# Kernel optimization log

Measured on AMD Instinct MI355X. Metric: run time of the kernel, lower is better.

Reference implementation:

```python
import jax, jax.numpy as jnp
import numpy as np

N = 400_000   # active voxels
CIN = 64
COUT = 64
D = 192       # dense bounding volume side
K = 27        # 3x3x3 kernel taps


def _build_kmap():
    """Build per-tap neighbor index map [27, N], -1 where neighbor voxel is inactive.
    Mirrors fvdb's SparseConvPackInfo for stride=1, kernel=3, out_grid == in_grid."""
    rng = np.random.default_rng(0)
    coords = rng.integers(0, D, size=(int(N * 1.6), 3), dtype=np.int64)
    lin = coords[:, 0] * D * D + coords[:, 1] * D + coords[:, 2]
    lin = np.unique(lin)[:N]
    assert lin.shape[0] == N
    coords = np.stack([lin // (D * D), (lin // D) % D, lin % D], axis=1)
    lookup = np.full(D * D * D, -1, np.int32)
    lookup[lin] = np.arange(N, dtype=np.int32)
    nbr = np.full((K, N), -1, np.int32)
    k = 0
    for a in (-1, 0, 1):
        for b in (-1, 0, 1):
            for c in (-1, 0, 1):
                nc = coords + np.array([a, b, c])
                valid = np.all((nc >= 0) & (nc < D), axis=1)
                nlin = nc[:, 0] * D * D + nc[:, 1] * D + nc[:, 2]
                nbr[k, valid] = lookup[nlin[valid]]
                k += 1
    return jnp.asarray(nbr)


def setup_inputs() -> dict:
    key = jax.random.key(0)
    k1, k2, k3 = jax.random.split(key, 3)
    std = 1.0 / np.sqrt(CIN * K)  # reset_parameters: uniform(-std, std)
    feats = jax.random.normal(k1, (N, CIN), jnp.float32)
    weight = jax.random.uniform(k2, (K, CIN, COUT), jnp.float32, -std, std)
    bias = jax.random.uniform(k3, (COUT,), jnp.float32, -std, std)
    return {"feats": feats, "weight": weight, "bias": bias, "nbr_idx": _build_kmap()}


def reference(feats, weight, bias, nbr_idx):
    # Gather-scatter sparse conv: out[j] = bias + sum_k feats[nbr_k(j)] @ W[k]
    safe_idx = jnp.maximum(nbr_idx, 0)          # [K, N]
    valid = nbr_idx >= 0                        # [K, N]
    out0 = jnp.broadcast_to(bias, (N, COUT)).astype(feats.dtype)

    def tap(carry, xs):
        idx, msk, w = xs                        # [N], [N], [CIN, COUT]
        g = jnp.where(msk[:, None], feats[idx], 0.0)  # masked gather [N, CIN]
        return carry + g @ w, None

    out, _ = jax.lax.scan(tap, out0, (safe_idx, valid, weight))
    return out
```

## Files before the change

### kernel.cpp

```cpp
#include <hip/hip_runtime.h>
#include <stdint.h>

#define NVOX 400000
#define KTAPS 27

typedef __bf16 bf16x8 __attribute__((ext_vector_type(8)));
typedef float floatx16 __attribute__((ext_vector_type(16)));

__device__ __forceinline__ uint32_t f2bf(float f) {
  uint32_t u = __builtin_bit_cast(uint32_t, f);
  u += 0x7fffu + ((u >> 16) & 1u);
  return u >> 16;
}

__device__ __forceinline__ floatx16 zero16() {
  floatx16 z = {0.f,0.f,0.f,0.f,0.f,0.f,0.f,0.f,
                0.f,0.f,0.f,0.f,0.f,0.f,0.f,0.f};
  return z;
}

__global__ void k_wt(const float* __restrict__ W, unsigned short* __restrict__ Wt) {
  int i = blockIdx.x * 256 + threadIdx.x;
  int k = i >> 12;
  int rem = i & 4095;
  int ci = rem >> 6;
  int co = rem & 63;
  Wt[(k << 12) + (co << 6) + ci] = (unsigned short)f2bf(W[i]);
}

__global__ void k_feats(const float4* __restrict__ F, uint2* __restrict__ Fb) {
  int i0 = blockIdx.x * 1024 + threadIdx.x;
#pragma unroll
  for (int j = 0; j < 4; ++j) {
    int i = i0 + j * 256;
    float4 v = F[i];
    uint2 o;
    o.x = f2bf(v.x) | (f2bf(v.y) << 16);
    o.y = f2bf(v.z) | (f2bf(v.w) << 16);
    Fb[i] = o;
  }
}

template<bool FB>
__global__ __launch_bounds__(256, 3) void k_conv(
    const float* __restrict__ feats,
    const unsigned short* __restrict__ featsb,
    const unsigned short* __restrict__ Wt,
    const float* __restrict__ bias,
    const int* __restrict__ nbr,
    float* __restrict__ out) {

  __shared__ alignas(16) unsigned short lA[256 * 72];
  __shared__ alignas(16) unsigned short lB[64 * 72];

  const int t = threadIdx.x;
  const int w = t >> 6;
  const int l = t & 63;
  const int half = l >> 5;
  const int lm = l & 31;
  const int v0 = blockIdx.x * 256;

  floatx16 acc00 = zero16(), acc01 = zero16(), acc10 = zero16(), acc11 = zero16();

  const unsigned short* pA0 = &lA[(w * 64 + lm) * 72 + half * 8];
  const unsigned short* pA1 = pA0 + 32 * 72;
  const unsigned short* pB0 = &lB[lm * 72 + half * 8];
  const unsigned short* pB1 = pB0 + 32 * 72;

  const int rr = t >> 3;
  const int cc = t & 7;

  int voff[8];
  bool vld[8];
#pragma unroll
  for (int p = 0; p < 8; ++p) {
    voff[p] = v0 + p * 32 + rr;
    vld[p] = voff[p] < NVOX;
  }
  const int brow = t >> 2;
  const int bcol = (t & 3) * 16;

  int idxA[8];
  int idxN[8];
  uint4 rA[8];
  uint4 rB0, rB1;

  auto gather = [&](int id) -> uint4 {
    int sid = id < 0 ? 0 : id;
    if (FB) {
      return *(const uint4*)(featsb + (size_t)sid * 64 + cc * 8);
    } else {
      const float* s = feats + (size_t)sid * 64 + cc * 8;
      float4 f0 = *(const float4*)s;
      float4 f1 = *(const float4*)(s + 4);
      uint4 d;
      d.x = f2bf(f0.x) | (f2bf(f0.y) << 16);
      d.y = f2bf(f0.z) | (f2bf(f0.w) << 16);
      d.z = f2bf(f1.x) | (f2bf(f1.y) << 16);
      d.w = f2bf(f1.z) | (f2bf(f1.w) << 16);
      return d;
    }
  };

#pragma unroll
  for (int p = 0; p < 8; ++p) idxN[p] = vld[p] ? nbr[voff[p]] : -1;
  {
    const unsigned short* src = Wt + brow * 64 + bcol;
    rB0 = *(const uint4*)src;
    rB1 = *(const uint4*)(src + 8);
  }
#pragma unroll
  for (int p = 0; p < 8; ++p) {
    int id = idxN[p];
    idxA[p] = id;
    rA[p] = gather(id);
  }
#pragma unroll
  for (int p = 0; p < 8; ++p) idxN[p] = vld[p] ? nbr[NVOX + voff[p]] : -1;

#pragma unroll 1
  for (int k = 0; k < KTAPS; ++k) {
    __syncthreads();

#pragma unroll
    for (int p = 0; p < 8; ++p) {
      uint4 v = rA[p];
      if (idxA[p] < 0) { v.x = 0u; v.y = 0u; v.z = 0u; v.w = 0u; }
      *(uint4*)&lA[(p * 32 + rr) * 72 + cc * 8] = v;
    }
    {
      unsigned short* dst = &lB[brow * 72 + bcol];
      *(uint4*)dst = rB0;
      *(uint4*)(dst + 8) = rB1;
    }
    __syncthreads();

    if (k + 1 < KTAPS) {
      const unsigned short* src = Wt + ((k + 1) << 12) + brow * 64 + bcol;
      rB0 = *(const uint4*)src;
      rB1 = *(const uint4*)(src + 8);
#pragma unroll
      for (int p = 0; p < 8; ++p) {
        int id = idxN[p];
        idxA[p] = id;
        rA[p] = gather(id);
      }
      if (k + 2 < KTAPS) {
        const int* nb = nbr + (size_t)(k + 2) * NVOX;
#pragma unroll
        for (int p = 0; p < 8; ++p) idxN[p] = vld[p] ? nb[voff[p]] : -1;
      }
    }

#pragma unroll
    for (int kc = 0; kc < 4; ++kc) {
      bf16x8 a0 = *(const bf16x8*)(pA0 + kc * 16);
      bf16x8 a1 = *(const bf16x8*)(pA1 + kc * 16);
      bf16x8 b0 = *(const bf16x8*)(pB0 + kc * 16);
      bf16x8 b1 = *(const bf16x8*)(pB1 + kc * 16);
      acc00 = __builtin_amdgcn_mfma_f32_32x32x16_bf16(a0, b0, acc00, 0, 0, 0);
      acc01 = __builtin_amdgcn_mfma_f32_32x32x16_bf16(a0, b1, acc01, 0, 0, 0);
      acc10 = __builtin_amdgcn_mfma_f32_32x32x16_bf16(a1, b0, acc10, 0, 0, 0);
      acc11 = __builtin_amdgcn_mfma_f32_32x32x16_bf16(a1, b1, acc11, 0, 0, 0);
    }
  }

  float bv0 = bias[lm];
  float bv1 = bias[32 + lm];
#pragma unroll
  for (int reg = 0; reg < 16; ++reg) {
    int m = (reg & 3) + 8 * (reg >> 2) + 4 * half;
    int vm0 = v0 + w * 64 + m;
    int vm1 = vm0 + 32;
    if (vm0 < NVOX) {
      out[vm0 * 64 + lm]      = acc00[reg] + bv0;
      out[vm0 * 64 + 32 + lm] = acc01[reg] + bv1;
    }
    if (vm1 < NVOX) {
      out[vm1 * 64 + lm]      = acc10[reg] + bv0;
      out[vm1 * 64 + 32 + lm] = acc11[reg] + bv1;
    }
  }
}

extern "C" void kernel_launch(void* const* d_in, const int* in_sizes, int n_in,
                              void* d_out, int out_size, void* d_ws, size_t ws_size,
                              hipStream_t stream) {
  const float* feats  = (const float*)d_in[0];
  const float* weight = (const float*)d_in[1];
  const float* bias   = (const float*)d_in[2];
  const int*   nbr    = (const int*)d_in[3];
  float* out = (float*)d_out;

  unsigned short* Wt = (unsigned short*)d_ws;
  const size_t featsOff = 256 * 1024;
  const size_t fbytes = (size_t)NVOX * 64 * 2;
  const bool bigws = ws_size >= featsOff + fbytes;

  k_wt<<<432, 256, 0, stream>>>(weight, Wt);

  const int grid = (NVOX + 255) / 256;
  if (bigws) {
    unsigned short* Fb = (unsigned short*)((char*)d_ws + featsOff);
    k_feats<<<6250, 256, 0, stream>>>((const float4*)feats, (uint2*)Fb);
    k_conv<true><<<grid, 256, 0, stream>>>(feats, Fb, Wt, bias, nbr, out);
  } else {
    k_conv<false><<<grid, 256, 0, stream>>>(feats, nullptr, Wt, bias, nbr, out);
  }
}
```

Before: 357.8 us.

## Compact valid neighbor pairs per tile and run MFMA only on active chunks

Each 128-voxel tile now ballots the 27 neighbor-map rows and builds a compacted list of valid (row, neighbor) pairs in LDS, split into 16-row chunks per tap. Only these chunks are gathered and multiplied with small 16x16x32 MFMAs, and results are scatter-added into an LDS accumulator. This avoids gathering and multiplying the many inactive neighbors that the dense per-tap tiling processed. It also drops the separate bf16 feature-conversion prepass and remaps block IDs across XCDs. The cost is two barriers per small chunk, scattered LDS adds, and a hard cap on pairs per tile.

```diff
diff --git a/kernel.cpp b/kernel.cpp
--- a/kernel.cpp
+++ b/kernel.cpp
@@ -3,20 +3,17 @@
 
 #define NVOX 400000
 #define KTAPS 27
+#define TILE 128
+#define CAP 1024
+#define NCHUNK_CAP (CAP / 16 + KTAPS)
 
 typedef __bf16 bf16x8 __attribute__((ext_vector_type(8)));
-typedef float floatx16 __attribute__((ext_vector_type(16)));
+typedef float floatx4 __attribute__((ext_vector_type(4)));
 
 __device__ __forceinline__ uint32_t f2bf(float f) {
   uint32_t u = __builtin_bit_cast(uint32_t, f);
   u += 0x7fffu + ((u >> 16) & 1u);
   return u >> 16;
-}
-
-__device__ __forceinline__ floatx16 zero16() {
-  floatx16 z = {0.f,0.f,0.f,0.f,0.f,0.f,0.f,0.f,
-                0.f,0.f,0.f,0.f,0.f,0.f,0.f,0.f};
-  return z;
 }
 
 __global__ void k_wt(const float* __restrict__ W, unsigned short* __restrict__ Wt) {
@@ -28,69 +25,94 @@
   Wt[(k << 12) + (co << 6) + ci] = (unsigned short)f2bf(W[i]);
 }
 
-__global__ void k_feats(const float4* __restrict__ F, uint2* __restrict__ Fb) {
-  int i0 = blockIdx.x * 1024 + threadIdx.x;
-#pragma unroll
-  for (int j = 0; j < 4; ++j) {
-    int i = i0 + j * 256;
-    float4 v = F[i];
-    uint2 o;
-    o.x = f2bf(v.x) | (f2bf(v.y) << 16);
-    o.y = f2bf(v.z) | (f2bf(v.w) << 16);
-    Fb[i] = o;
-  }
-}
-
-template<bool FB>
 __global__ __launch_bounds__(256, 3) void k_conv(
     const float* __restrict__ feats,
-    const unsigned short* __restrict__ featsb,
     const unsigned short* __restrict__ Wt,
     const float* __restrict__ bias,
     const int* __restrict__ nbr,
     float* __restrict__ out) {
 
-  __shared__ alignas(16) unsigned short lA[256 * 72];
-  __shared__ alignas(16) unsigned short lB[64 * 72];
+  __shared__ float accS[4 * TILE * 16];
+  __shared__ alignas(16) unsigned short lA[2][16 * 72];
+  __shared__ int pairIdx[CAP];
+  __shared__ unsigned short pairRow[CAP];
+  __shared__ unsigned long long masksS[KTAPS * 2];
+  __shared__ int woff[KTAPS * 2 + 1];
+  __shared__ unsigned int chunkTab[NCHUNK_CAP];
+  __shared__ int nChunksS;
 
   const int t = threadIdx.x;
   const int w = t >> 6;
   const int l = t & 63;
-  const int half = l >> 5;
-  const int lm = l & 31;
-  const int v0 = blockIdx.x * 256;
-
-  floatx16 acc00 = zero16(), acc01 = zero16(), acc10 = zero16(), acc11 = zero16();
-
-  const unsigned short* pA0 = &lA[(w * 64 + lm) * 72 + half * 8];
-  const unsigned short* pA1 = pA0 + 32 * 72;
-  const unsigned short* pB0 = &lB[lm * 72 + half * 8];
-  const unsigned short* pB1 = pB0 + 32 * 72;
+
+  const int nwg = gridDim.x;
+  const int q = nwg >> 3, r8 = nwg & 7;
+  const int xcd = blockIdx.x & 7, hi = blockIdx.x >> 3;
+  const int wg = (xcd < r8 ? xcd * (q + 1) : r8 * (q + 1) + (xcd - r8) * q) + hi;
+  const int v0 = wg * TILE;
+
+  {
+    float4 z = make_float4(0.f, 0.f, 0.f, 0.f);
+    float4* a4 = (float4*)accS;
+#pragma unroll
+    for (int i = 0; i < 8; ++i) a4[t + i * 256] = z;
+  }
+
+#pragma unroll
+  for (int k = 0; k < KTAPS; ++k) {
+    int id = (t < TILE) ? nbr[(size_t)k * NVOX + v0 + t] : -1;
+    unsigned long long m = __ballot(id >= 0);
+    if (l == 0 && w < 2) masksS[k * 2 + w] = m;
+  }
+  __syncthreads();
+  if (w == 0) {
+    int c = (l < KTAPS * 2) ? __popcll(masksS[l]) : 0;
+#pragma unroll
+    for (int d = 1; d < 64; d <<= 1) { int o = __shfl_up(c, d); if (l >= d) c += o; }
+    if (l < KTAPS * 2) woff[l + 1] = c;
+    if (l == 0) woff[0] = 0;
+  }
+  __syncthreads();
+#pragma unroll
+  for (int k = 0; k < KTAPS; ++k) {
+    int id = (t < TILE) ? nbr[(size_t)k * NVOX + v0 + t] : -1;
+    if (id >= 0) {
+      unsigned long long m = masksS[k * 2 + w];
+      int pos = woff[k * 2 + w] + __popcll(m & ((1ull << l) - 1ull));
+      if (pos < CAP) { pairRow[pos] = (unsigned short)t; pairIdx[pos] = id; }
+    }
+  }
+  if (w == 0) {
+    int b0 = 0, cnt = 0;
+    if (l < KTAPS) {
+      b0 = min(woff[2 * l], CAP);
+      cnt = min(woff[2 * l + 2], CAP) - b0;
+    }
+    int nch = (cnt + 15) >> 4;
+    int inc = nch;
+#pragma unroll
+    for (int d = 1; d < 64; d <<= 1) { int o = __shfl_up(inc, d); if (l >= d) inc += o; }
+    int base = inc - nch;
+    for (int j = 0; j < nch; ++j) {
+      int st = b0 + 16 * j;
+      int ln = min(16, cnt - 16 * j);
+      chunkTab[base + j] = ((unsigned)l << 16) | ((unsigned)st << 5) | (unsigned)ln;
+    }
+    if (l == KTAPS - 1) nChunksS = inc;
+  }
+  __syncthreads();
+  const int nc = nChunksS;
 
   const int rr = t >> 3;
-  const int cc = t & 7;
-
-  int voff[8];
-  bool vld[8];
-#pragma unroll
-  for (int p = 0; p < 8; ++p) {
-    voff[p] = v0 + p * 32 + rr;
-    vld[p] = voff[p] < NVOX;
-  }
-  const int brow = t >> 2;
-  const int bcol = (t & 3) * 16;
-
-  int idxA[8];
-  int idxN[8];
-  uint4 rA[8];
-  uint4 rB0, rB1;
-
-  auto gather = [&](int id) -> uint4 {
-    int sid = id < 0 ? 0 : id;
-    if (FB) {
-      return *(const uint4*)(featsb + (size_t)sid * 64 + cc * 8);
-    } else {
-      const float* s = feats + (size_t)sid * 64 + cc * 8;
+  const int jc = t & 7;
+
+  auto gatherA = [&](unsigned int meta, uint4& sreg, bool& svalid) {
+    int st = (meta >> 5) & 0x7FF;
+    int ln = (int)(meta & 31u);
+    svalid = (t < TILE) && (rr < ln);
+    if (svalid) {
+      int idx = pairIdx[st + rr];
+      const float* s = feats + (size_t)idx * 64 + jc * 8;
       float4 f0 = *(const float4*)s;
       float4 f1 = *(const float4*)(s + 4);
       uint4 d;
@@ -98,87 +120,91 @@
       d.y = f2bf(f0.z) | (f2bf(f0.w) << 16);
       d.z = f2bf(f1.x) | (f2bf(f1.y) << 16);
       d.w = f2bf(f1.z) | (f2bf(f1.w) << 16);
-      return d;
+      sreg = d;
     }
   };
-
-#pragma unroll
-  for (int p = 0; p < 8; ++p) idxN[p] = vld[p] ? nbr[voff[p]] : -1;
+  auto bload = [&](int k, uint4& b0, uint4& b1) {
+    const unsigned short* src = Wt + (k << 12) + (w * 16 + (l & 15)) * 64 + ((l >> 4) * 8);
+    b0 = *(const uint4*)src;
+    b1 = *(const uint4*)(src + 32);
+  };
+
+  unsigned int mCur = 0, mNxt = 0;
+  uint4 sA0, sA1;
+  bool sV0 = false, sV1 = false;
+  uint4 rB0, rB1;
+
+  if (nc > 0) {
+    mCur = chunkTab[0];
+    gatherA(mCur, sA0, sV0);
+    bload((int)(mCur >> 16), rB0, rB1);
+  }
+  if (nc > 1) {
+    mNxt = chunkTab[1];
+    gatherA(mNxt, sA1, sV1);
+  }
+
+#pragma unroll 1
+  for (int c = 0; c < nc; ++c) {
+    __syncthreads();
+    {
+      bool sv = (c & 1) ? sV1 : sV0;
+      uint4 v = (c & 1) ? sA1 : sA0;
+      if (sv) *(uint4*)&lA[c & 1][rr * 72 + jc * 8] = v;
+    }
+    __syncthreads();
+
+    const int kCur = (int)(mCur >> 16);
+    const int stCur = (int)((mCur >> 5) & 0x7FF);
+    const int lnCur = (int)(mCur & 31u);
+
+    unsigned int mNew = 0;
+    if (c + 2 < nc) {
+      mNew = chunkTab[c + 2];
+      if ((c & 1) == 0) gatherA(mNew, sA0, sV0);
+      else              gatherA(mNew, sA1, sV1);
+    } else {
+      if ((c & 1) == 0) sV0 = false; else sV1 = false;
+    }
+    uint4 nB0 = rB0, nB1 = rB1;
+    if (c + 1 < nc) {
+      int kN = (int)(mNxt >> 16);
+      if (kN != kCur) bload(kN, nB0, nB1);
+    }
+
+    const unsigned short* aB = &lA[c & 1][(l & 15) * 72 + ((l >> 4) * 8)];
+    bf16x8 a0 = *(const bf16x8*)aB;
+    bf16x8 a1 = *(const bf16x8*)(aB + 32);
+    floatx4 d = {0.f, 0.f, 0.f, 0.f};
+    d = __builtin_amdgcn_mfma_f32_16x16x32_bf16(a0, __builtin_bit_cast(bf16x8, rB0), d, 0, 0, 0);
+    d = __builtin_amdgcn_mfma_f32_16x16x32_bf16(a1, __builtin_bit_cast(bf16x8, rB1), d, 0, 0, 0);
+
+    float* slab = accS + w * (TILE * 16) + (l & 15);
+#pragma unroll
+    for (int j2 = 0; j2 < 4; ++j2) {
+      int r2 = (l >> 4) * 4 + j2;
+      if (r2 < lnCur) {
+        int tr = pairRow[stCur + r2];
+        slab[tr * 16] += d[j2];
+      }
+    }
+
+    mCur = mNxt; mNxt = mNew; rB0 = nB0; rB1 = nB1;
+  }
+
+  __syncthreads();
   {
-    const unsigned short* src = Wt + brow * 64 + bcol;
-    rB0 = *(const uint4*)src;
-    rB1 = *(const uint4*)(src + 8);
-  }
-#pragma unroll
-  for (int p = 0; p < 8; ++p) {
-    int id = idxN[p];
-    idxA[p] = id;
-    rA[p] = gather(id);
-  }
-#pragma unroll
-  for (int p = 0; p < 8; ++p) idxN[p] = vld[p] ? nbr[NVOX + voff[p]] : -1;
-
-#pragma unroll 1
-  for (int k = 0; k < KTAPS; ++k) {
-    __syncthreads();
-
-#pragma unroll
-    for (int p = 0; p < 8; ++p) {
-      uint4 v = rA[p];
-      if (idxA[p] < 0) { v.x = 0u; v.y = 0u; v.z = 0u; v.w = 0u; }
-      *(uint4*)&lA[(p * 32 + rr) * 72 + cc * 8] = v;
-    }
-    {
-      unsigned short* dst = &lB[brow * 72 + bcol];
-      *(uint4*)dst = rB0;
-      *(uint4*)(dst + 8) = rB1;
-    }
-    __syncthreads();
-
-    if (k + 1 < KTAPS) {
-      const unsigned short* src = Wt + ((k + 1) << 12) + brow * 64 + bcol;
-      rB0 = *(const uint4*)src;
-      rB1 = *(const uint4*)(src + 8);
-#pragma unroll
-      for (int p = 0; p < 8; ++p) {
-        int id = idxN[p];
-        idxA[p] = id;
-        rA[p] = gather(id);
-      }
-      if (k + 2 < KTAPS) {
-        const int* nb = nbr + (size_t)(k + 2) * NVOX;
-#pragma unroll
-        for (int p = 0; p < 8; ++p) idxN[p] = vld[p] ? nb[voff[p]] : -1;
-      }
-    }
-
-#pragma unroll
-    for (int kc = 0; kc < 4; ++kc) {
-      bf16x8 a0 = *(const bf16x8*)(pA0 + kc * 16);
-      bf16x8 a1 = *(const bf16x8*)(pA1 + kc * 16);
-      bf16x8 b0 = *(const bf16x8*)(pB0 + kc * 16);
-      bf16x8 b1 = *(const bf16x8*)(pB1 + kc * 16);
-      acc00 = __builtin_amdgcn_mfma_f32_32x32x16_bf16(a0, b0, acc00, 0, 0, 0);
-      acc01 = __builtin_amdgcn_mfma_f32_32x32x16_bf16(a0, b1, acc01, 0, 0, 0);
-      acc10 = __builtin_amdgcn_mfma_f32_32x32x16_bf16(a1, b0, acc10, 0, 0, 0);
-      acc11 = __builtin_amdgcn_mfma_f32_32x32x16_bf16(a1, b1, acc11, 0, 0, 0);
-    }
-  }
-
-  float bv0 = bias[lm];
-  float bv1 = bias[32 + lm];
-#pragma unroll
-  for (int reg = 0; reg < 16; ++reg) {
-    int m = (reg & 3) + 8 * (reg >> 2) + 4 * half;
-    int vm0 = v0 + w * 64 + m;
-    int vm1 = vm0 + 32;
-    if (vm0 < NVOX) {
-      out[vm0 * 64 + lm]      = acc00[reg] + bv0;
-      out[vm0 * 64 + 32 + lm] = acc01[reg] + bv1;
-    }
-    if (vm1 < NVOX) {
-      out[vm1 * 64 + lm]      = acc10[reg] + bv0;
-      out[vm1 * 64 + 32 + lm] = acc11[reg] + bv1;
+    int vox = t >> 1;
+    int cb = (t & 1) * 32;
+    float* op = out + (size_t)(v0 + vox) * 64 + cb;
+#pragma unroll
+    for (int qq = 0; qq < 8; ++qq) {
+      int c0 = cb + qq * 4;
+      const float* ap = accS + (c0 >> 4) * (TILE * 16) + vox * 16 + (c0 & 15);
+      float4 v = *(const float4*)ap;
+      float4 bv = *(const float4*)(bias + c0);
+      v.x += bv.x; v.y += bv.y; v.z += bv.z; v.w += bv.w;
+      *(float4*)(op + qq * 4) = v;
     }
   }
 }
@@ -193,18 +219,7 @@
   float* out = (float*)d_out;
 
   unsigned short* Wt = (unsigned short*)d_ws;
-  const size_t featsOff = 256 * 1024;
-  const size_t fbytes = (size_t)NVOX * 64 * 2;
-  const bool bigws = ws_size >= featsOff + fbytes;
 
   k_wt<<<432, 256, 0, stream>>>(weight, Wt);
-
-  const int grid = (NVOX + 255) / 256;
-  if (bigws) {
-    unsigned short* Fb = (unsigned short*)((char*)d_ws + featsOff);
-    k_feats<<<6250, 256, 0, stream>>>((const float4*)feats, (uint2*)Fb);
-    k_conv<true><<<grid, 256, 0, stream>>>(feats, Fb, Wt, bias, nbr, out);
-  } else {
-    k_conv<false><<<grid, 256, 0, stream>>>(feats, nullptr, Wt, bias, nbr, out);
-  }
-}
+  k_conv<<<NVOX / TILE, 256, 0, stream>>>(feats, Wt, bias, nbr, out);
+}
```

After: 478.3 us. +33.7%, slower.
